# Kernel optimization log

Measured on AMD Instinct MI355X. Metric: run time of the kernel, lower is better.

The kernel has to match this reference:

```python
import jax, jax.numpy as jnp
import numpy as np

E = 8            # n_experts
TEMP = float(np.e)
N_ACTIVE = 5     # max(1, int(8 * 0.7))
EPS = 1e-8


def setup_inputs() -> dict:
    key = jax.random.key(0)
    ks = jax.random.split(key, 6)
    N, D, H, O = 8192, 1024, 2048, 1024

    def init(k, shape, fan_in):
        return (jax.random.normal(k, shape, jnp.float32) / np.sqrt(fan_in)).astype(jnp.float32)

    return {
        "x": jax.random.normal(ks[0], (N, D), jnp.float32),
        "gate_W": init(ks[1], (D, E), D),
        "gate_b": jnp.zeros((E,), jnp.float32),
        "W1": init(ks[2], (E, D, H), D),
        "b1": jnp.zeros((E, H), jnp.float32),
        "W2": init(ks[3], (E, H, H), H),
        "b2": jnp.zeros((E, H), jnp.float32),
        "W3": init(ks[4], (E, H, O), H),
        "b3": jnp.zeros((E, O), jnp.float32),
    }


def reference(x, gate_W, gate_b, W1, b1, W2, b2, W3, b3):
    # Boltzmann gate: softmax(scores / T), keep top n_active, renormalize.
    scores = (x @ gate_W + gate_b) / TEMP            # [N, E]
    probs = jax.nn.softmax(scores, axis=-1)          # [N, E]
    _, idx = jax.lax.top_k(probs, N_ACTIVE)          # [N, n_active]
    rows = jnp.arange(probs.shape[0])[:, None]
    mask = jnp.zeros_like(probs).at[rows, idx].set(1.0)
    w = probs * mask
    w = w / (w.sum(axis=-1, keepdims=True) + EPS)    # [N, E]

    # Dense all-expert MLP (dropout is identity in eval mode).
    h = jax.nn.relu(jnp.einsum('nd,edh->enh', x, W1) + b1[:, None, :])   # [E, N, H]
    h = jax.nn.relu(jnp.einsum('enh,ehk->enk', h, W2) + b2[:, None, :])  # [E, N, H]
    out = jnp.einsum('enh,eho->eno', h, W3) + b3[:, None, :]             # [E, N, O]

    # Weighted combine over experts.
    return jnp.einsum('ne,eno->no', w, out)          # [N, O]
```

## Files before the change

### kernel.cpp

```cpp
#include <hip/hip_runtime.h>

#define N_ROWS 8192
#define DIM_D  1024
#define DIM_H  2048
#define DIM_O  1024
#define NEXP   8
#define NACT   5
#define MT128  336

typedef _Float16 f16x8 __attribute__((ext_vector_type(8)));
typedef _Float16 f16x4 __attribute__((ext_vector_type(4)));
typedef float    f32x4 __attribute__((ext_vector_type(4)));

__device__ __forceinline__ void gload_lds16(const void* g, void* l) {
  __builtin_amdgcn_global_load_lds(
      (const __attribute__((address_space(1))) void*)g,
      (__attribute__((address_space(3))) void*)l, 16, 0, 0);
}

__global__ void convert_x_kernel(const float* __restrict__ in,
                                 _Float16* __restrict__ out, int n) {
  int i = (blockIdx.x * 256 + threadIdx.x) * 8;
  if (i >= n) return;
  const float4 a = *(const float4*)(in + i);
  const float4 b = *(const float4*)(in + i + 4);
  f16x8 v;
  v[0] = (_Float16)a.x; v[1] = (_Float16)a.y; v[2] = (_Float16)a.z; v[3] = (_Float16)a.w;
  v[4] = (_Float16)b.x; v[5] = (_Float16)b.y; v[6] = (_Float16)b.z; v[7] = (_Float16)b.w;
  *(f16x8*)(out + i) = v;
}

__global__ void zero_f32_kernel(float* __restrict__ p, int n4) {
  int i = blockIdx.x * 256 + threadIdx.x;
  if (i < n4) ((float4*)p)[i] = make_float4(0.f, 0.f, 0.f, 0.f);
}
__global__ void zero_counts_kernel(int* __restrict__ cnt) {
  if (threadIdx.x < NEXP) cnt[threadIdx.x] = 0;
}

__global__ void transpose_to_f16(const float* __restrict__ in,
                                 _Float16* __restrict__ out, int R, int C) {
  in  += (size_t)blockIdx.z * R * C;
  out += (size_t)blockIdx.z * R * C;
  __shared__ float tile[32][33];
  const int tx = threadIdx.x & 31, ty = threadIdx.x >> 5;
  const int c0 = blockIdx.x * 32, r0 = blockIdx.y * 32;
#pragma unroll
  for (int j = 0; j < 32; j += 8)
    tile[ty + j][tx] = in[(size_t)(r0 + ty + j) * C + c0 + tx];
  __syncthreads();
  const int cc = threadIdx.x >> 3;
  const int r4 = (threadIdx.x & 7) * 4;
  f16x4 v;
#pragma unroll
  for (int i = 0; i < 4; ++i) v[i] = (_Float16)tile[r4 + i][cc];
  *(f16x4*)(out + (size_t)(c0 + cc) * R + r0 + r4) = v;
}

__global__ void gate_kernel(const float* __restrict__ x, const float* __restrict__ gW,
                            const float* __restrict__ gb, float* __restrict__ wout) {
  const int lane = threadIdx.x & 63;
  const int row  = blockIdx.x * 4 + (threadIdx.x >> 6);
  float acc[8] = {0.f,0.f,0.f,0.f,0.f,0.f,0.f,0.f};
  const float* xr = x + (size_t)row * DIM_D;
  for (int d = lane; d < DIM_D; d += 64) {
    float xv = xr[d];
    const float4* g4 = (const float4*)(gW + d * 8);
    float4 a = g4[0], b = g4[1];
    acc[0] += xv * a.x; acc[1] += xv * a.y; acc[2] += xv * a.z; acc[3] += xv * a.w;
    acc[4] += xv * b.x; acc[5] += xv * b.y; acc[6] += xv * b.z; acc[7] += xv * b.w;
  }
#pragma unroll
  for (int off = 32; off > 0; off >>= 1) {
#pragma unroll
    for (int e = 0; e < 8; ++e) acc[e] += __shfl_xor(acc[e], off);
  }
  const float invT = 0.36787944117144233f;
  float s[8], mx = -1e30f;
#pragma unroll
  for (int e = 0; e < 8; ++e) { s[e] = (acc[e] + gb[e]) * invT; mx = fmaxf(mx, s[e]); }
  float p[8], sum = 0.f;
#pragma unroll
  for (int e = 0; e < 8; ++e) { p[e] = expf(s[e] - mx); sum += p[e]; }
  float inv = 1.f / sum;
#pragma unroll
  for (int e = 0; e < 8; ++e) p[e] *= inv;
  unsigned keep = 0;
  for (int it = 0; it < NACT; ++it) {
    int best = 0; float bv = -1.f;
#pragma unroll
    for (int e = 0; e < 8; ++e)
      if (!(keep & (1u << e)) && p[e] > bv) { bv = p[e]; best = e; }
    keep |= 1u << best;
  }
  float ks = 0.f;
#pragma unroll
  for (int e = 0; e < 8; ++e) if (keep & (1u << e)) ks += p[e];
  const float winv = 1.f / (ks + 1e-8f);
  if (lane < 8)
    wout[(size_t)row * 8 + lane] = (keep & (1u << lane)) ? p[lane] * winv : 0.f;
}

__global__ void count_kernel(const float* __restrict__ wg, int* __restrict__ cnt) {
  const int row = blockIdx.x * 256 + threadIdx.x;
  const int lane = threadIdx.x & 63;
#pragma unroll
  for (int e = 0; e < NEXP; ++e) {
    const bool keep = wg[(size_t)row * 8 + e] > 0.f;
    unsigned long long m = __ballot(keep);
    if (lane == 0 && m) atomicAdd(&cnt[e], __popcll(m));
  }
}

__global__ void offsets_kernel(const int* __restrict__ cnt, int* __restrict__ cursor,
                               int* __restrict__ offs, int* __restrict__ ntiles,
                               int2* __restrict__ ttab, int* __restrict__ rlist) {
  __shared__ int soffs[NEXP], scnt[NEXP];
  if (threadIdx.x == 0) {
    int off = 0, k = 0;
    for (int e = 0; e < NEXP; ++e) {
      offs[e] = off; soffs[e] = off; scnt[e] = cnt[e];
      cursor[e] = 0;
      const int nt = (cnt[e] + 127) >> 7;
      for (int t2 = 0; t2 < nt; ++t2) { ttab[k] = make_int2(e, off + t2 * 128); ++k; }
      off += nt << 7;
    }
    *ntiles = k;
  }
  __syncthreads();
#pragma unroll
  for (int e = 0; e < NEXP; ++e) {
    const int lo = soffs[e] + scnt[e];
    const int hi = soffs[e] + ((scnt[e] + 127) & ~127);
    for (int i = lo + (int)threadIdx.x; i < hi; i += 256) rlist[i] = 0;
  }
}

__global__ void place_kernel(const float* __restrict__ wg, const int* __restrict__ offs,
                             int* __restrict__ cursor, int* __restrict__ rlist,
                             int* __restrict__ pos) {
  const int row = blockIdx.x * 256 + threadIdx.x;
  const int lane = threadIdx.x & 63;
#pragma unroll
  for (int e = 0; e < NEXP; ++e) {
    const bool keep = wg[(size_t)row * 8 + e] > 0.f;
    unsigned long long m = __ballot(keep);
    if (m) {
      const int leader = __ffsll(m) - 1;
      const int pre = __popcll(m & ((1ull << lane) - 1ull));
      int base = 0;
      if (lane == leader) base = atomicAdd(&cursor[e], __popcll(m));
      base = __shfl(base, leader);
      if (keep) {
        const int idx = offs[e] + base + pre;
        rlist[idx] = row;
        pos[(size_t)row * 8 + e] = idx;
      }
    }
  }
}

__global__ void combine_kernel(const float* __restrict__ wg, const int* __restrict__ pos,
                               const _Float16* __restrict__ y, float* __restrict__ out) {
  const int tid = blockIdx.x * 256 + threadIdx.x;
  const int row = tid >> 7, c8 = (tid & 127) * 8;
  float a[8] = {0.f,0.f,0.f,0.f,0.f,0.f,0.f,0.f};
#pragma unroll
  for (int e = 0; e < NEXP; ++e) {
    const float w = wg[(size_t)row * 8 + e];
    if (w > 0.f) {
      const int p = pos[(size_t)row * 8 + e];
      const f16x8 v = *(const f16x8*)(y + (size_t)p * DIM_O + c8);
#pragma unroll
      for (int j = 0; j < 8; ++j) a[j] += w * (float)v[j];
    }
  }
  float4* o4 = (float4*)(out + (size_t)row * DIM_O + c8);
  o4[0] = make_float4(a[0], a[1], a[2], a[3]);
  o4[1] = make_float4(a[4], a[5], a[6], a[7]);
}

#define MFMA16 __builtin_amdgcn_mfma_f32_16x16x32_f16
template <int MODE>
__global__ __launch_bounds__(256, 4) void gemm128(
    const _Float16* __restrict__ A, const _Float16* __restrict__ BtAll,
    _Float16* __restrict__ C, const float* __restrict__ biasAll,
    const int* __restrict__ rlist, const int2* __restrict__ ttab,
    const int* __restrict__ ntilesp, int N, int K) {
  const int ncol = gridDim.x;
  const int b = blockIdx.y * ncol + blockIdx.x;
  const int xcd = b & 7, idx = b >> 3;
  const int ti = xcd * (MT128 / 8) + idx / ncol;
  const int colt = idx % ncol;
  if (ti >= *ntilesp) return;
  const int2 tt = ttab[ti];
  const int e = tt.x, grow0 = tt.y;
  const int col0 = colt * 128;

  __shared__ _Float16 sA[128 * 64];
  __shared__ _Float16 sB[128 * 64];
  const int t = threadIdx.x;
  const int w = t >> 6, lane = t & 63;
  const int wm = w >> 1, wn = w & 1;
  const int l15 = lane & 15, lg = lane >> 4;

  const _Float16* Bt = BtAll + (size_t)e * N * K;

  const int cb = (((t & 7) ^ ((t >> 3) & 7))) * 8;
  size_t arow[4], brow[4];
#pragma unroll
  for (int i = 0; i < 4; ++i) {
    const int chunk = i * 256 + t;
    const int r = chunk >> 3;
    const int gr = (MODE == 0) ? rlist[grow0 + r] : (grow0 + r);
    arow[i] = (size_t)gr * K;
    brow[i] = (size_t)(col0 + r) * K;
  }

  const int ck0 = ((lg * 16) ^ ((l15 & 7) << 4)) >> 1;
  const int ck1 = ((64 + lg * 16) ^ ((l15 & 7) << 4)) >> 1;

  f32x4 acc[4][4] = {};

  for (int kt = 0; kt < K; kt += 64) {
    __syncthreads();
#pragma unroll
    for (int i = 0; i < 4; ++i)
      gload_lds16(A + arow[i] + kt + cb, sA + (i * 256 + w * 64) * 8);
#pragma unroll
    for (int i = 0; i < 4; ++i)
      gload_lds16(Bt + brow[i] + kt + cb, sB + (i * 256 + w * 64) * 8);
    __syncthreads();
#pragma unroll
    for (int k2 = 0; k2 < 2; ++k2) {
      const int ck = k2 ? ck1 : ck0;
      f16x8 af[4], bf[4];
#pragma unroll
      for (int m = 0; m < 4; ++m)
        af[m] = *(const f16x8*)(sA + (wm * 64 + m * 16 + l15) * 64 + ck);
#pragma unroll
      for (int n = 0; n < 4; ++n)
        bf[n] = *(const f16x8*)(sB + (wn * 64 + n * 16 + l15) * 64 + ck);
#pragma unroll
      for (int m = 0; m < 4; ++m)
#pragma unroll
        for (int n = 0; n < 4; ++n)
          acc[m][n] = MFMA16(af[m], bf[n], acc[m][n], 0, 0, 0);
    }
  }

  const float* bias = biasAll + (size_t)e * N;
#pragma unroll
  for (int m = 0; m < 4; ++m) {
#pragma unroll
    for (int n = 0; n < 4; ++n) {
      const int gc = col0 + wn * 64 + n * 16 + l15;
      const float bv = bias[gc];
#pragma unroll
      for (int r = 0; r < 4; ++r) {
        const int grow = grow0 + wm * 64 + m * 16 + lg * 4 + r;
        const float v = acc[m][n][r] + bv;
        C[(size_t)grow * N + gc] = (_Float16)((MODE == 2) ? v : fmaxf(v, 0.f));
      }
    }
  }
}

__global__ void compact_old(const float* __restrict__ wg, int* __restrict__ cnt,
                            int* __restrict__ rowlist) {
  const int row = blockIdx.x * 256 + threadIdx.x;
  const int lane = threadIdx.x & 63;
#pragma unroll
  for (int e = 0; e < NEXP; ++e) {
    const float w = wg[(size_t)row * 8 + e];
    const bool keep = (w > 0.f);
    unsigned long long m = __ballot(keep);
    if (m) {
      const int leader = __ffsll(m) - 1;
      const int pre = __popcll(m & ((1ull << lane) - 1ull));
      int base = 0;
      if (lane == leader) base = atomicAdd(&cnt[e], __popcll(m));
      base = __shfl(base, leader);
      if (keep) rowlist[e * N_ROWS + base + pre] = row;
    }
  }
}

template <int MODE>
__global__ __launch_bounds__(256, 2) void gemm_nt(
    const _Float16* __restrict__ A, const _Float16* __restrict__ Bt,
    void* __restrict__ Cout, const float* __restrict__ bias,
    const float* __restrict__ wg, const int* __restrict__ rlist,
    const int* __restrict__ cntp, int e, int N, int K) {
  const int M = *cntp;
  const int row0 = blockIdx.y * 128, col0 = blockIdx.x * 128;
  if (row0 >= M) return;
  __shared__ _Float16 sA[128 * 64];
  __shared__ _Float16 sB[128 * 64];
  const int t = threadIdx.x;
  const int w = t >> 6, lane = t & 63;
  const int wm = w >> 1, wn = w & 1;
  const int l15 = lane & 15, lg = lane >> 4;
  size_t arow[4];
#pragma unroll
  for (int i = 0; i < 4; ++i) {
    const int chunk = i * 256 + t;
    int li = row0 + (chunk >> 3);
    if (li >= M && MODE == 0) li = M - 1;
    const int gr = (MODE == 0) ? rlist[li] : li;
    arow[i] = (size_t)gr * K;
  }
  f32x4 acc[4][4] = {};
  for (int kt = 0; kt < K; kt += 64) {
    __syncthreads();
#pragma unroll
    for (int i = 0; i < 4; ++i) {
      const int chunk = i * 256 + t;
      const int cb = (chunk & 7) * 8;
      gload_lds16(A + arow[i] + kt + cb, sA + (i * 256 + w * 64) * 8);
    }
#pragma unroll
    for (int i = 0; i < 4; ++i) {
      const int chunk = i * 256 + t;
      const int r = chunk >> 3, cb = (chunk & 7) * 8;
      gload_lds16(Bt + (size_t)(col0 + r) * K + kt + cb, sB + (i * 256 + w * 64) * 8);
    }
    __syncthreads();
#pragma unroll
    for (int k2 = 0; k2 < 2; ++k2) {
      f16x8 af[4], bf[4];
#pragma unroll
      for (int m = 0; m < 4; ++m)
        af[m] = *(const f16x8*)(sA + (wm * 64 + m * 16 + l15) * 64 + k2 * 32 + lg * 8);
#pragma unroll
      for (int n = 0; n < 4; ++n)
        bf[n] = *(const f16x8*)(sB + (wn * 64 + n * 16 + l15) * 64 + k2 * 32 + lg * 8);
#pragma unroll
      for (int m = 0; m < 4; ++m)
#pragma unroll
        for (int n = 0; n < 4; ++n)
          acc[m][n] = MFMA16(af[m], bf[n], acc[m][n], 0, 0, 0);
    }
  }
#pragma unroll
  for (int m = 0; m < 4; ++m) {
#pragma unroll
    for (int n = 0; n < 4; ++n) {
      const int gc = col0 + wn * 64 + n * 16 + l15;
      const float bvv = bias[gc];
#pragma unroll
      for (int r = 0; r < 4; ++r) {
        const int gr = row0 + wm * 64 + m * 16 + lg * 4 + r;
        float v = acc[m][n][r] + bvv;
        if (MODE == 3) {
          if (gr < M) {
            const int orow = rlist[gr];
            atomicAdd((float*)Cout + (size_t)orow * N + gc,
                      wg[(size_t)orow * 8 + e] * v);
          }
        } else {
          ((_Float16*)Cout)[(size_t)gr * N + gc] = (_Float16)fmaxf(v, 0.f);
        }
      }
    }
  }
}

extern "C" void kernel_launch(void* const* d_in, const int* in_sizes, int n_in,
                              void* d_out, int out_size, void* d_ws, size_t ws_size,
                              hipStream_t stream) {
  const float* x  = (const float*)d_in[0];
  const float* gW = (const float*)d_in[1];
  const float* gb = (const float*)d_in[2];
  const float* W1 = (const float*)d_in[3];
  const float* b1 = (const float*)d_in[4];
  const float* W2 = (const float*)d_in[5];
  const float* b2 = (const float*)d_in[6];
  const float* W3 = (const float*)d_in[7];
  const float* b3 = (const float*)d_in[8];
  float* out = (float*)d_out;

  char* ws = (char*)d_ws;
  const bool big = (ws_size >= 0x1E100000ULL);

  if (big) {
    float* wgate   = (float*)ws;
    int*   meta    = (int*)(ws + 0x40000);
    int*   cnt     = meta;
    int*   cursor  = meta + 8;
    int*   offs    = meta + 16;
    int*   ntiles  = meta + 24;
    int2*  ttab    = (int2*)(meta + 32);
    int*   pos     = (int*)(ws + 0x80000);
    int*   rlistg  = (int*)(ws + 0xC0000);
    _Float16* xh   = (_Float16*)(ws + 0x100000);
    _Float16* h1   = (_Float16*)(ws + 0x1100000);
    _Float16* h2   = (_Float16*)(ws + 0xB900000);
    _Float16* wt1  = (_Float16*)(ws + 0x16100000);
    _Float16* wt2  = (_Float16*)(ws + 0x18100000);
    _Float16* wt3  = (_Float16*)(ws + 0x1C100000);
    _Float16* y    = h1;

    convert_x_kernel<<<(N_ROWS * DIM_D) / (256 * 8), 256, 0, stream>>>(x, xh, N_ROWS * DIM_D);
    gate_kernel<<<N_ROWS / 4, 256, 0, stream>>>(x, gW, gb, wgate);
    zero_counts_kernel<<<1, 64, 0, stream>>>(cnt);
    count_kernel<<<N_ROWS / 256, 256, 0, stream>>>(wgate, cnt);
    offsets_kernel<<<1, 256, 0, stream>>>(cnt, cursor, offs, ntiles, ttab, rlistg);
    place_kernel<<<N_ROWS / 256, 256, 0, stream>>>(wgate, offs, cursor, rlistg, pos);

    transpose_to_f16<<<dim3(DIM_H / 32, DIM_D / 32, NEXP), 256, 0, stream>>>(W1, wt1, DIM_D, DIM_H);
    transpose_to_f16<<<dim3(DIM_H / 32, DIM_H / 32, NEXP), 256, 0, stream>>>(W2, wt2, DIM_H, DIM_H);
    transpose_to_f16<<<dim3(DIM_O / 32, DIM_H / 32, NEXP), 256, 0, stream>>>(W3, wt3, DIM_H, DIM_O);

    gemm128<0><<<dim3(DIM_H / 128, MT128), 256, 0, stream>>>(
        xh, wt1, h1, b1, rlistg, ttab, ntiles, DIM_H, DIM_D);
    gemm128<1><<<dim3(DIM_H / 128, MT128), 256, 0, stream>>>(
        h1, wt2, h2, b2, rlistg, ttab, ntiles, DIM_H, DIM_H);
    gemm128<2><<<dim3(DIM_O / 128, MT128), 256, 0, stream>>>(
        h2, wt3, y, b3, rlistg, ttab, ntiles, DIM_O, DIM_H);

    combine_kernel<<<(N_ROWS * 128) / 256, 256, 0, stream>>>(wgate, pos, y, out);
  } else {
    float*    wgate = (float*)ws;
    int*      cnt   = (int*)(ws + 0x40000);
    int*      rlist = (int*)(ws + 0x80000);
    _Float16* xh    = (_Float16*)(ws + 0x100000);
    _Float16* h1    = (_Float16*)(ws + 0x1100000);
    _Float16* h2    = (_Float16*)(ws + 0x3100000);
    _Float16* wt1   = (_Float16*)(ws + 0x5100000);
    _Float16* wt2   = (_Float16*)(ws + 0x5500000);
    _Float16* wt3   = (_Float16*)(ws + 0x5D00000);

    convert_x_kernel<<<(N_ROWS * DIM_D) / (256 * 8), 256, 0, stream>>>(x, xh, N_ROWS * DIM_D);
    gate_kernel<<<N_ROWS / 4, 256, 0, stream>>>(x, gW, gb, wgate);
    zero_counts_kernel<<<1, 64, 0, stream>>>(cnt);
    compact_old<<<N_ROWS / 256, 256, 0, stream>>>(wgate, cnt, rlist);
    zero_f32_kernel<<<(N_ROWS * DIM_O / 4 + 255) / 256, 256, 0, stream>>>(out, N_ROWS * DIM_O / 4);

    for (int e = 0; e < NEXP; ++e) {
      transpose_to_f16<<<dim3(DIM_H / 32, DIM_D / 32, 1), 256, 0, stream>>>(
          W1 + (size_t)e * DIM_D * DIM_H, wt1, DIM_D, DIM_H);
      transpose_to_f16<<<dim3(DIM_H / 32, DIM_H / 32, 1), 256, 0, stream>>>(
          W2 + (size_t)e * DIM_H * DIM_H, wt2, DIM_H, DIM_H);
      transpose_to_f16<<<dim3(DIM_O / 32, DIM_H / 32, 1), 256, 0, stream>>>(
          W3 + (size_t)e * DIM_H * DIM_O, wt3, DIM_H, DIM_O);
      const int* ce = cnt + e;
      const int* re = rlist + e * N_ROWS;
      gemm_nt<0><<<dim3(DIM_H / 128, N_ROWS / 128), 256, 0, stream>>>(
          xh, wt1, h1, b1 + (size_t)e * DIM_H, wgate, re, ce, e, DIM_H, DIM_D);
      gemm_nt<1><<<dim3(DIM_H / 128, N_ROWS / 128), 256, 0, stream>>>(
          h1, wt2, h2, b2 + (size_t)e * DIM_H, wgate, re, ce, e, DIM_H, DIM_H);
      gemm_nt<3><<<dim3(DIM_O / 128, N_ROWS / 128), 256, 0, stream>>>(
          h2, wt3, out, b3 + (size_t)e * DIM_O, wgate, re, ce, e, DIM_O, DIM_H);
    }
  }
}
```

Measured before the change: 887.7 us.

## Double-buffer GEMM LDS tiles with K=32 stages and explicit waitcnt pipelining

The single-buffer K=64 tile loop in gemm128 becomes a two-stage double-buffered pipeline with K=32 tiles. The next-next tile's global-to-LDS loads are issued right after fragments are read into registers, so the loads overlap the MFMA work. Explicit vmcnt/lgkmcnt waits, sched barriers and setprio around the MFMA block control the ordering, and a new XOR swizzle on row pairs is meant to avoid LDS bank conflicts. The cost is twice as many barrier pairs per unit of K and a shallower MFMA batch per iteration.

```diff
diff --git a/kernel.cpp b/kernel.cpp
--- a/kernel.cpp
+++ b/kernel.cpp
@@ -11,6 +11,8 @@
 typedef _Float16 f16x8 __attribute__((ext_vector_type(8)));
 typedef _Float16 f16x4 __attribute__((ext_vector_type(4)));
 typedef float    f32x4 __attribute__((ext_vector_type(4)));
+
+#define SB __builtin_amdgcn_sched_barrier(0)
 
 __device__ __forceinline__ void gload_lds16(const void* g, void* l) {
   __builtin_amdgcn_global_load_lds(
@@ -197,8 +199,8 @@
   const int e = tt.x, grow0 = tt.y;
   const int col0 = colt * 128;
 
-  __shared__ _Float16 sA[128 * 64];
-  __shared__ _Float16 sB[128 * 64];
+  __shared__ _Float16 sA[2][128 * 32];
+  __shared__ _Float16 sB[2][128 * 32];
   const int t = threadIdx.x;
   const int w = t >> 6, lane = t & 63;
   const int wm = w >> 1, wn = w & 1;
@@ -206,47 +208,68 @@
 
   const _Float16* Bt = BtAll + (size_t)e * N * K;
 
-  const int cb = (((t & 7) ^ ((t >> 3) & 7))) * 8;
-  size_t arow[4], brow[4];
-#pragma unroll
-  for (int i = 0; i < 4; ++i) {
-    const int chunk = i * 256 + t;
-    const int r = chunk >> 3;
-    const int gr = (MODE == 0) ? rlist[grow0 + r] : (grow0 + r);
-    arow[i] = (size_t)gr * K;
-    brow[i] = (size_t)(col0 + r) * K;
-  }
-
-  const int ck0 = ((lg * 16) ^ ((l15 & 7) << 4)) >> 1;
-  const int ck1 = ((64 + lg * 16) ^ ((l15 & 7) << 4)) >> 1;
+  size_t asrc[2], bsrc[2];
+  int ldsL[2];
+#pragma unroll
+  for (int u = 0; u < 2; ++u) {
+    const int L = u * 256 + t;
+    const int rp = L >> 3, s = L & 7;
+    const int x = s ^ (rp & 7);
+    const int row = rp * 2 + (x >> 2), g = x & 3;
+    const int gr = (MODE == 0) ? rlist[grow0 + row] : (grow0 + row);
+    asrc[u] = (size_t)gr * K + g * 8;
+    bsrc[u] = (size_t)(col0 + row) * K + g * 8;
+    ldsL[u] = L * 8;
+  }
+
+  const int sofs = ((lg + 4 * (l15 & 1)) ^ (l15 >> 1)) * 8;
+  int rpA[4], rpB[4];
+#pragma unroll
+  for (int m = 0; m < 4; ++m) rpA[m] = ((wm * 64 + m * 16 + l15) >> 1) * 64;
+#pragma unroll
+  for (int n = 0; n < 4; ++n) rpB[n] = ((wn * 64 + n * 16 + l15) >> 1) * 64;
+
+  auto STAGE = [&](int tile, int sbuf) {
+    const int kofs = tile * 32;
+#pragma unroll
+    for (int u = 0; u < 2; ++u)
+      gload_lds16(A + asrc[u] + kofs, &sA[sbuf][ldsL[u]]);
+#pragma unroll
+    for (int u = 0; u < 2; ++u)
+      gload_lds16(Bt + bsrc[u] + kofs, &sB[sbuf][ldsL[u]]);
+  };
 
   f32x4 acc[4][4] = {};
-
-  for (int kt = 0; kt < K; kt += 64) {
-    __syncthreads();
-#pragma unroll
-    for (int i = 0; i < 4; ++i)
-      gload_lds16(A + arow[i] + kt + cb, sA + (i * 256 + w * 64) * 8);
-#pragma unroll
-    for (int i = 0; i < 4; ++i)
-      gload_lds16(Bt + brow[i] + kt + cb, sB + (i * 256 + w * 64) * 8);
-    __syncthreads();
-#pragma unroll
-    for (int k2 = 0; k2 < 2; ++k2) {
-      const int ck = k2 ? ck1 : ck0;
-      f16x8 af[4], bf[4];
-#pragma unroll
-      for (int m = 0; m < 4; ++m)
-        af[m] = *(const f16x8*)(sA + (wm * 64 + m * 16 + l15) * 64 + ck);
+  const int NT = K >> 5;
+
+  STAGE(0, 0);
+  STAGE(1, 1);
+
+  for (int tk = 0; tk < NT; ++tk) {
+    const int buf = tk & 1;
+    if (tk + 1 < NT) asm volatile("s_waitcnt vmcnt(4)" ::: "memory");
+    else             asm volatile("s_waitcnt vmcnt(0)" ::: "memory");
+    SB; __builtin_amdgcn_s_barrier(); SB;
+
+    f16x8 af[4], bf[4];
+#pragma unroll
+    for (int m = 0; m < 4; ++m)
+      af[m] = *(const f16x8*)(&sA[buf][rpA[m] + sofs]);
+#pragma unroll
+    for (int n = 0; n < 4; ++n)
+      bf[n] = *(const f16x8*)(&sB[buf][rpB[n] + sofs]);
+    asm volatile("s_waitcnt lgkmcnt(0)" ::: "memory");
+    SB; __builtin_amdgcn_s_barrier(); SB;
+
+    if (tk + 2 < NT) STAGE(tk + 2, buf);
+
+    __builtin_amdgcn_s_setprio(1);
+#pragma unroll
+    for (int m = 0; m < 4; ++m)
 #pragma unroll
       for (int n = 0; n < 4; ++n)
-        bf[n] = *(const f16x8*)(sB + (wn * 64 + n * 16 + l15) * 64 + ck);
-#pragma unroll
-      for (int m = 0; m < 4; ++m)
-#pragma unroll
-        for (int n = 0; n < 4; ++n)
-          acc[m][n] = MFMA16(af[m], bf[n], acc[m][n], 0, 0, 0);
-    }
+        acc[m][n] = MFMA16(af[m], bf[n], acc[m][n], 0, 0, 0);
+    __builtin_amdgcn_s_setprio(0);
   }
 
   const float* bias = biasAll + (size_t)e * N;
```

Result: slower. 1.021 ms (+15.0%).
